# Kernel tuning notes

Hardware: AMD Instinct MI355X
Metric: run time of the kernel (lower is better)

Reference implementation:

```python
import jax, jax.numpy as jnp
import numpy as np

B, T, D = 4, 2048, 2048
H = 16
HO = D // H  # head_out = 128


def setup_inputs() -> dict:
    key = jax.random.key(0)
    ks = jax.random.split(key, 6)
    x = jax.random.normal(ks[0], (B, T, D), dtype=jnp.float32)
    scale = 0.02
    Wq = jax.random.normal(ks[1], (D, D), dtype=jnp.float32) * scale
    Wk = jax.random.normal(ks[2], (D, D), dtype=jnp.float32) * scale
    Wv = jax.random.normal(ks[3], (D, D), dtype=jnp.float32) * scale
    Wp = jax.random.normal(ks[4], (D, D), dtype=jnp.float32) * scale
    bp = jnp.zeros((D,), dtype=jnp.float32)
    return {"x": x, "Wq": Wq, "Wk": Wk, "Wv": Wv, "Wp": Wp, "bp": bp}


def reference(x, Wq, Wk, Wv, Wp, bp):
    b, t, _ = x.shape
    # QKV projections (weights stored [d_in, d_out])
    q = x @ Wq
    k = x @ Wk
    v = x @ Wv
    split = lambda a: a.reshape(b, t, H, HO).transpose(0, 2, 1, 3)  # [b,H,T,ho]
    qh, kh, vh = split(q), split(k), split(v)
    # Feature attention: contract over tokens -> [b,H,ho,ho]
    scores = jnp.einsum('bhtf,bhtg->bhfg', qh, kh) / jnp.sqrt(jnp.float32(HO))
    weights = jax.nn.softmax(scores, axis=-1)  # dropout p=0.0 (identity)
    # feature_alibi: [1/T, 1/(T-1), ..., 1], broadcast over batch/head/feature
    feat_alibi = (1.0 / jnp.arange(t, 0, -1, dtype=jnp.float32)).reshape(1, 1, t, 1)
    vh = vh + feat_alibi
    # (weights @ v^T)^T : ctx[b,h,t,f] = sum_g weights[b,h,f,g] * v[b,h,t,g]
    ctx = jnp.einsum('bhfg,bhtg->bhtf', weights, vh)
    ctx = ctx.transpose(0, 2, 1, 3).reshape(b, t, H * HO)  # [b,T,d_out]
    return ctx @ Wp + bp
```

## Files before the change

### kernel.cpp

```cpp
#include <hip/hip_runtime.h>
#include <hip/hip_bf16.h>


#define Tt 2048
#define Dd 2048
#define Mm 8192

typedef __attribute__((ext_vector_type(4))) float f32x4;
typedef __attribute__((ext_vector_type(8))) short s16x8;
static_assert(sizeof(s16x8) == 16, "frag size");

typedef const __attribute__((address_space(1))) void* gptr_t;
typedef __attribute__((address_space(3))) void* lptr_t;

__device__ __forceinline__ float bf2f(ushort u) {
    union { unsigned int i; float f; } c; c.i = ((unsigned int)u) << 16; return c.f;
}
__device__ __forceinline__ ushort f2bf(float f) {
    union { float f; unsigned int i; } c; c.f = f;
    return (ushort)((c.i + 0x7FFFu + ((c.i >> 16) & 1u)) >> 16);
}
__device__ __forceinline__ void gload16(const void* g, void* l) {
    __builtin_amdgcn_global_load_lds((gptr_t)g, (lptr_t)l, 16, 0, 0);
}
__device__ __forceinline__ s16x8 ldfrag(const char* p) { return *(const s16x8*)p; }

#define MFMA_BF16(d, a, b) \
    asm("v_mfma_f32_16x16x32_bf16 %0, %1, %2, %0" : "+v"(d) : "v"(a), "v"(b))


__global__ __launch_bounds__(256) void convx_kernel(const float* __restrict__ x,
                                                    ushort* __restrict__ xb) {
    const int idx = blockIdx.x * 256 + threadIdx.x;
    const int stride = gridDim.x * 256;
    for (int i = idx; i < Mm * Dd / 4; i += stride) {
        const float4 v = *(const float4*)(x + (size_t)i * 4);
        ushort4 o; o.x = f2bf(v.x); o.y = f2bf(v.y); o.z = f2bf(v.z); o.w = f2bf(v.w);
        *(ushort4*)(xb + (size_t)i * 4) = o;
    }
}

__global__ __launch_bounds__(256) void transw_kernel(const float* __restrict__ W0,
        const float* __restrict__ W1, const float* __restrict__ W2,
        const float* __restrict__ W3, ushort* __restrict__ Wt) {
    __shared__ float tile[64][65];
    const int z = blockIdx.z;
    const float* W = (z == 0) ? W0 : (z == 1) ? W1 : (z == 2) ? W2 : W3;
    ushort* dst = Wt + (size_t)z * ((size_t)Dd * Dd);
    const int n0 = blockIdx.x * 64, k0 = blockIdx.y * 64;
    const int r4 = threadIdx.x >> 6, c = threadIdx.x & 63;
#pragma unroll
    for (int i = 0; i < 16; i++) {
        const int row = i * 4 + r4;
        tile[row][c] = W[(size_t)(k0 + row) * Dd + n0 + c];
    }
    __syncthreads();
#pragma unroll
    for (int i = 0; i < 16; i++) {
        const int row = i * 4 + r4;
        dst[(size_t)(n0 + row) * Dd + k0 + c] = f2bf(tile[c][row]);
    }
}


__device__ __forceinline__ void stage_half(char* ldsRegion, const ushort* gRegion,
                                           int ld, int half, int tid) {
#pragma unroll
    for (int j = 0; j < 2; j++) {
        const int Pb = half * 16384 + j * 8192 + (tid >> 6) * 1024;
        const int P = Pb + (tid & 63) * 16;
        const int row = P >> 7;
        const int colb = (P ^ ((row & 7) << 4)) & 127;
        gload16(gRegion + (size_t)row * ld + (colb >> 1), ldsRegion + Pb);
    }
}

template <int MODE>
__global__ __launch_bounds__(512, 2) void gemm256_kernel(
        const ushort* __restrict__ A, const ushort* __restrict__ Bt,
        void* __restrict__ Cv, const float* __restrict__ bias,
        int Kdim, int lda, int ldb, int ldc,
        size_t bstride, size_t cstride) {
    extern __shared__ char lds[];

    const int tid = threadIdx.x;
    const int lane = tid & 63;
    const int w = tid >> 6;
    const int wr = w >> 2, wc = w & 3;
    const int fr = lane & 15, fq = lane >> 4;

    const int bid = blockIdx.x;
    const int wg = (bid & 7) * 32 + (bid >> 3);
    const int m0 = (wg >> 3) * 256;
    const int n0 = (wg & 7) * 256;

    const ushort* Ag = A + (size_t)m0 * lda;
    const ushort* Bg = Bt + (size_t)blockIdx.z * bstride + (size_t)n0 * ldb;
    const int NT = Kdim >> 6;

    const int aoff = wr * 16384 + fr * 128;
    const int boff = wc * 8192 + fr * 128;
    const int xo = (fr & 7) << 4;
    const int cp0 = (fq * 16) ^ xo;
    const int cp1 = (64 + fq * 16) ^ xo;

    f32x4 acc[8][4];
#pragma unroll
    for (int i = 0; i < 8; i++)
#pragma unroll
        for (int j = 0; j < 4; j++) acc[i][j] = {0.f, 0.f, 0.f, 0.f};

    s16x8 afX[4][2], afY[4][2], bf01[2][2], bf23[2][2];

    {
        char* b0 = lds;
        char* b1 = lds + 65536;
        stage_half(b0,         Ag, lda, 0, tid);
        stage_half(b0,         Ag, lda, 1, tid);
        stage_half(b0 + 32768, Bg, ldb, 0, tid);
        stage_half(b0 + 32768, Bg, ldb, 1, tid);
        if (NT > 1) {
            stage_half(b1, Ag + 64, lda, 0, tid);
            stage_half(b1, Ag + 64, lda, 1, tid);
        }
        __builtin_amdgcn_sched_barrier(0);
        if (NT > 1) asm volatile("s_waitcnt vmcnt(4)" ::: "memory");
        else        asm volatile("s_waitcnt vmcnt(0)" ::: "memory");
        __builtin_amdgcn_s_barrier();
        const char* Ab = b0 + aoff;
        const char* Bb = b0 + 32768 + boff;
#pragma unroll
        for (int m = 0; m < 4; m++) {
            afX[m][0] = ldfrag(Ab + m * 2048 + cp0);
            afX[m][1] = ldfrag(Ab + m * 2048 + cp1);
        }
#pragma unroll
        for (int n = 0; n < 2; n++) {
            bf01[n][0] = ldfrag(Bb + n * 2048 + cp0);
            bf01[n][1] = ldfrag(Bb + n * 2048 + cp1);
        }
        __builtin_amdgcn_sched_barrier(0);
    }

    for (int t = 0; t < NT; ++t) {
        char* bufc = lds + (t & 1) * 65536;
        char* bufn = lds + ((t & 1) ^ 1) * 65536;
        const char* Ab = bufc + aoff;
        const char* Bb = bufc + 32768 + boff;

#pragma unroll
        for (int n = 0; n < 2; n++) {
            bf23[n][0] = ldfrag(Bb + (n + 2) * 2048 + cp0);
            bf23[n][1] = ldfrag(Bb + (n + 2) * 2048 + cp1);
        }
        if (t + 1 < NT) stage_half(bufn + 32768, Bg + (size_t)(t + 1) * 64, ldb, 0, tid);
        __builtin_amdgcn_sched_barrier(0);
        __builtin_amdgcn_s_barrier();
        asm volatile("s_waitcnt lgkmcnt(4)" ::: "memory");
        __builtin_amdgcn_s_setprio(1);
#pragma unroll
        for (int k = 0; k < 2; k++)
#pragma unroll
            for (int m = 0; m < 4; m++)
#pragma unroll
                for (int n = 0; n < 2; n++) MFMA_BF16(acc[m][n], afX[m][k], bf01[n][k]);
        __builtin_amdgcn_s_setprio(0);
        __builtin_amdgcn_s_barrier();

#pragma unroll
        for (int m = 0; m < 4; m++) {
            afY[m][0] = ldfrag(Ab + (m + 4) * 2048 + cp0);
            afY[m][1] = ldfrag(Ab + (m + 4) * 2048 + cp1);
        }
        if (t + 1 < NT) stage_half(bufn + 32768, Bg + (size_t)(t + 1) * 64, ldb, 1, tid);
        __builtin_amdgcn_sched_barrier(0);
        __builtin_amdgcn_s_barrier();
        asm volatile("s_waitcnt lgkmcnt(8)" ::: "memory");
        __builtin_amdgcn_s_setprio(1);
#pragma unroll
        for (int k = 0; k < 2; k++)
#pragma unroll
            for (int m = 0; m < 4; m++)
#pragma unroll
                for (int n = 0; n < 2; n++) MFMA_BF16(acc[m][n + 2], afX[m][k], bf23[n][k]);
        __builtin_amdgcn_s_setprio(0);
        __builtin_amdgcn_s_barrier();

        asm volatile("s_waitcnt lgkmcnt(0)" ::: "memory");
        __builtin_amdgcn_s_setprio(1);
#pragma unroll
        for (int k = 0; k < 2; k++)
#pragma unroll
            for (int m = 0; m < 4; m++)
#pragma unroll
                for (int n = 0; n < 2; n++) MFMA_BF16(acc[m + 4][n], afY[m][k], bf01[n][k]);
        __builtin_amdgcn_s_setprio(0);
        __builtin_amdgcn_s_barrier();

        if (t + 2 < NT) {
            stage_half(bufc, Ag + (size_t)(t + 2) * 64, lda, 0, tid);
            stage_half(bufc, Ag + (size_t)(t + 2) * 64, lda, 1, tid);
        }
        __builtin_amdgcn_sched_barrier(0);
        if (t + 2 < NT) asm volatile("s_waitcnt vmcnt(4)" ::: "memory");
        else            asm volatile("s_waitcnt vmcnt(0)" ::: "memory");
        __builtin_amdgcn_s_barrier();
        if (t + 1 < NT) {
            const char* nAb = bufn + aoff;
            const char* nBb = bufn + 32768 + boff;
#pragma unroll
            for (int m = 0; m < 4; m++) {
                afX[m][0] = ldfrag(nAb + m * 2048 + cp0);
                afX[m][1] = ldfrag(nAb + m * 2048 + cp1);
            }
#pragma unroll
            for (int n = 0; n < 2; n++) {
                bf01[n][0] = ldfrag(nBb + n * 2048 + cp0);
                bf01[n][1] = ldfrag(nBb + n * 2048 + cp1);
            }
        }
        __builtin_amdgcn_sched_barrier(0);
        __builtin_amdgcn_s_setprio(1);
#pragma unroll
        for (int k = 0; k < 2; k++)
#pragma unroll
            for (int m = 0; m < 4; m++)
#pragma unroll
                for (int n = 0; n < 2; n++) MFMA_BF16(acc[m + 4][n + 2], afY[m][k], bf23[n][k]);
        __builtin_amdgcn_s_setprio(0);
        __builtin_amdgcn_s_barrier();
    }

    asm volatile("s_nop 7\ns_nop 7\ns_nop 7");

    if (MODE == 2) {
        float* C = (float*)Cv;
#pragma unroll
        for (int mi = 0; mi < 8; mi++)
#pragma unroll
            for (int ni = 0; ni < 4; ni++)
#pragma unroll
                for (int r = 0; r < 4; r++) {
                    const int row = m0 + wr * 128 + mi * 16 + fq * 4 + r;
                    const int col = n0 + wc * 64 + ni * 16 + fr;
                    C[(size_t)row * ldc + col] = acc[mi][ni][r] + bias[col];
                }
    } else {
        ushort* C = (ushort*)Cv + (size_t)blockIdx.z * cstride;
#pragma unroll
        for (int mi = 0; mi < 8; mi++)
#pragma unroll
            for (int ni = 0; ni < 4; ni++)
#pragma unroll
                for (int r = 0; r < 4; r++) {
                    const int row = m0 + wr * 128 + mi * 16 + fq * 4 + r;
                    const int col = n0 + wc * 64 + ni * 16 + fr;
                    C[(size_t)row * ldc + col] = f2bf(acc[mi][ni][r]);
                }
    }
}


template <int MODE>
__global__ __launch_bounds__(256, 2) void gemm_kernel(
        const ushort* __restrict__ A, const ushort* __restrict__ Bt,
        void* __restrict__ Cv, const float* __restrict__ bias,
        int Kdim, int lda, int ldb, int ldc) {
    __shared__ ushort lsA[128 * 32];
    __shared__ ushort lsB[128 * 32];

    const int tid = threadIdx.x;
    const int w = tid >> 6, lane = tid & 63;
    const int m0 = blockIdx.y * 128;
    const int n0 = blockIdx.x * 128;

    const ushort* Ab = A;
    const ushort* Bb = Bt;
    size_t coff = 0;
    if (MODE == 1) {
        const int z = blockIdx.z, b = z >> 4, h = z & 15;
        const size_t ao = (size_t)b * ((size_t)Tt * Dd) + (size_t)h * 128;
        Ab += ao; Bb += (size_t)z * (128 * 128); coff = ao;
    }

    const int sr = lane >> 2;
    const int sc = (lane & 3) * 8;
    const int c0 = w, c1 = w + 4;
    const int rA0 = c0 * 16 + sr, rA1 = c1 * 16 + sr;

    const int fr = lane & 15, fq = lane >> 4;
    const int wr = (w >> 1) * 64, wc = (w & 1) * 64;

    f32x4 acc[4][4];
#pragma unroll
    for (int i = 0; i < 4; i++)
#pragma unroll
        for (int j = 0; j < 4; j++) acc[i][j] = {0.f, 0.f, 0.f, 0.f};

    for (int kt = 0; kt < Kdim; kt += 32) {
        gload16(Ab + (size_t)(m0 + rA0) * lda + kt + sc, lsA + c0 * 512);
        gload16(Ab + (size_t)(m0 + rA1) * lda + kt + sc, lsA + c1 * 512);
        gload16(Bb + (size_t)(n0 + rA0) * ldb + kt + sc, lsB + c0 * 512);
        gload16(Bb + (size_t)(n0 + rA1) * ldb + kt + sc, lsB + c1 * 512);
        __syncthreads();

        s16x8 afrag[4], bfrag[4];
#pragma unroll
        for (int i = 0; i < 4; i++)
            afrag[i] = *(const s16x8*)(lsA + (wr + i * 16 + fr) * 32 + fq * 8);
#pragma unroll
        for (int j = 0; j < 4; j++)
            bfrag[j] = *(const s16x8*)(lsB + (wc + j * 16 + fr) * 32 + fq * 8);
#pragma unroll
        for (int i = 0; i < 4; i++)
#pragma unroll
            for (int j = 0; j < 4; j++)
                MFMA_BF16(acc[i][j], afrag[i], bfrag[j]);
        __syncthreads();
    }

    asm volatile("s_nop 7\ns_nop 7\ns_nop 7");

    {
        ushort* C = (ushort*)Cv + coff;
#pragma unroll
        for (int i = 0; i < 4; i++)
#pragma unroll
            for (int j = 0; j < 4; j++)
#pragma unroll
                for (int r = 0; r < 4; r++) {
                    const int row = m0 + wr + i * 16 + fq * 4 + r;
                    const int col = n0 + wc + j * 16 + fr;
                    float val = acc[i][j][r];
                    if (MODE == 1) val += 1.0f / (float)(Tt - row);
                    C[(size_t)row * ldc + col] = f2bf(val);
                }
    }
}


__global__ __launch_bounds__(256) void scores_kernel(const ushort* __restrict__ q,
        const ushort* __restrict__ k, float* __restrict__ part) {
    __shared__ float lsQ[32][128];
    __shared__ float lsK[32][128];
    const int tid = threadIdx.x;
    const int s = blockIdx.x, bh = blockIdx.y;
    const int b = bh >> 4, h = bh & 15;
    const size_t base = (size_t)b * ((size_t)Tt * Dd) + (size_t)h * 128;
    const ushort* qb = q + base;
    const ushort* kb = k + base;
    const int ty = tid >> 4, tx = tid & 15;
    const int f0 = ty * 8, g0 = tx * 8;

    float acc[8][8];
#pragma unroll
    for (int i = 0; i < 8; i++)
#pragma unroll
        for (int j = 0; j < 8; j++) acc[i][j] = 0.f;

    for (int ch = 0; ch < 8; ch++) {
        const int t0 = s * 256 + ch * 32;
#pragma unroll
        for (int ii = 0; ii < 4; ii++) {
            const int e = ii * 1024 + tid * 4;
            const int r = e >> 7, cc = e & 127;
            const size_t ga = (size_t)(t0 + r) * Dd + cc;
            const ushort4 v4 = *(const ushort4*)(qb + ga);
            f32x4 qf = {bf2f(v4.x), bf2f(v4.y), bf2f(v4.z), bf2f(v4.w)};
            *(f32x4*)&lsQ[r][cc] = qf;
            const ushort4 w4 = *(const ushort4*)(kb + ga);
            f32x4 kf = {bf2f(w4.x), bf2f(w4.y), bf2f(w4.z), bf2f(w4.w)};
            *(f32x4*)&lsK[r][cc] = kf;
        }
        __syncthreads();
#pragma unroll 4
        for (int tl = 0; tl < 32; tl++) {
            float qv[8], kv[8];
            *(f32x4*)&qv[0] = *(const f32x4*)&lsQ[tl][f0];
            *(f32x4*)&qv[4] = *(const f32x4*)&lsQ[tl][f0 + 4];
            *(f32x4*)&kv[0] = *(const f32x4*)&lsK[tl][g0];
            *(f32x4*)&kv[4] = *(const f32x4*)&lsK[tl][g0 + 4];
#pragma unroll
            for (int i = 0; i < 8; i++)
#pragma unroll
                for (int j = 0; j < 8; j++)
                    acc[i][j] = fmaf(qv[i], kv[j], acc[i][j]);
        }
        __syncthreads();
    }
    float* pb = part + ((size_t)s * 64 + bh) * 16384;
#pragma unroll
    for (int i = 0; i < 8; i++) {
        f32x4 o0 = {acc[i][0], acc[i][1], acc[i][2], acc[i][3]};
        f32x4 o1 = {acc[i][4], acc[i][5], acc[i][6], acc[i][7]};
        *(f32x4*)&pb[(f0 + i) * 128 + g0] = o0;
        *(f32x4*)&pb[(f0 + i) * 128 + g0 + 4] = o1;
    }
}


__global__ __launch_bounds__(256) void softmax_kernel(const float* __restrict__ part,
                                                      ushort* __restrict__ wts) {
    const int tid = threadIdx.x;
    const int wv = tid >> 6, lane = tid & 63;
    const int row = blockIdx.x * 4 + wv;
    const float* p = part + (size_t)row * 128 + lane * 2;
    float v0 = 0.f, v1 = 0.f;
#pragma unroll
    for (int s = 0; s < 8; s++) {
        const float2 t = *(const float2*)(p + (size_t)s * 1048576);
        v0 += t.x; v1 += t.y;
    }
    const float sc = 0.088388347648318447f;
    v0 *= sc; v1 *= sc;
    float m = fmaxf(v0, v1);
#pragma unroll
    for (int off = 32; off > 0; off >>= 1) m = fmaxf(m, __shfl_xor(m, off));
    const float e0 = __expf(v0 - m), e1 = __expf(v1 - m);
    float smv = e0 + e1;
#pragma unroll
    for (int off = 32; off > 0; off >>= 1) smv += __shfl_xor(smv, off);
    const float inv = 1.0f / smv;
    ushort2 o; o.x = f2bf(e0 * inv); o.y = f2bf(e1 * inv);
    *(ushort2*)(wts + (size_t)row * 128 + lane * 2) = o;
}


extern "C" void kernel_launch(void* const* d_in, const int* in_sizes, int n_in,
                              void* d_out, int out_size, void* d_ws, size_t ws_size,
                              hipStream_t stream) {
    const float* x  = (const float*)d_in[0];
    const float* Wq = (const float*)d_in[1];
    const float* Wk = (const float*)d_in[2];
    const float* Wv = (const float*)d_in[3];
    const float* Wp = (const float*)d_in[4];
    const float* bp = (const float*)d_in[5];
    float* out = (float*)d_out;
    char* ws = (char*)d_ws;

    ushort* xb   = (ushort*)(ws);
    ushort* Wt   = (ushort*)(ws + (33ull << 20));
    ushort* q    = (ushort*)(ws + (65ull << 20));
    ushort* k    = (ushort*)(ws + (97ull << 20));
    ushort* v    = (ushort*)(ws + (129ull << 20));
    float*  part = (float*) (ws + (161ull << 20));
    ushort* wts  = (ushort*)(ws + (193ull << 20));
    ushort* ctx  = xb;

    const size_t WSZ = (size_t)Dd * Dd;
    const size_t QSTRIDE = (32ull << 20) / 2;

    static_cast<void>(hipFuncSetAttribute((const void*)gemm256_kernel<0>,
        hipFuncAttributeMaxDynamicSharedMemorySize, 131072));
    static_cast<void>(hipFuncSetAttribute((const void*)gemm256_kernel<2>,
        hipFuncAttributeMaxDynamicSharedMemorySize, 131072));

    convx_kernel<<<2048, 256, 0, stream>>>(x, xb);
    transw_kernel<<<dim3(32, 32, 4), 256, 0, stream>>>(Wq, Wk, Wv, Wp, Wt);

    gemm256_kernel<0><<<dim3(256, 1, 3), 512, 131072, stream>>>(
        xb, Wt, q, nullptr, 2048, 2048, 2048, 2048, WSZ, QSTRIDE);

    scores_kernel<<<dim3(8, 64), 256, 0, stream>>>(q, k, part);
    softmax_kernel<<<2048, 256, 0, stream>>>(part, wts);

    gemm_kernel<1><<<dim3(1, 16, 64), 256, 0, stream>>>(v, wts, ctx, nullptr, 128, 2048, 128, 2048);

    gemm256_kernel<2><<<dim3(256, 1, 1), 512, 131072, stream>>>(
        ctx, Wt + 3 * WSZ, out, bp, 2048, 2048, 2048, 2048, 0, 0);
}
```

Baseline: 370.6 us.

## Restructure GEMM main loop to prefetch both A and B two tiles ahead

Changes the software pipeline of the bf16 MFMA GEMM so that both A and B tiles are staged into LDS two iterations ahead, instead of prefetching B only one iteration ahead. The per-iteration fragment loads for afX/bf01 move to the top of the loop rather than being issued at the end of the previous iteration. The vmcnt waits are adjusted to match the deeper prefetch. The aim is to hide more global-load latency. The cost is less overlap between LDS fragment reads and the MFMA blocks, since there are extra lgkmcnt(0) waits and barriers.

Result: no change. 376.8 us (+1.7%).

```diff
diff --git a/kernel.cpp b/kernel.cpp
--- a/kernel.cpp
+++ b/kernel.cpp
@@ -120,15 +120,24 @@
         stage_half(b0 + 32768, Bg, ldb, 0, tid);
         stage_half(b0 + 32768, Bg, ldb, 1, tid);
         if (NT > 1) {
-            stage_half(b1, Ag + 64, lda, 0, tid);
-            stage_half(b1, Ag + 64, lda, 1, tid);
-        }
-        __builtin_amdgcn_sched_barrier(0);
-        if (NT > 1) asm volatile("s_waitcnt vmcnt(4)" ::: "memory");
+            stage_half(b1,         Ag + 64, lda, 0, tid);
+            stage_half(b1,         Ag + 64, lda, 1, tid);
+            stage_half(b1 + 32768, Bg + 64, ldb, 0, tid);
+            stage_half(b1 + 32768, Bg + 64, ldb, 1, tid);
+        }
+        __builtin_amdgcn_sched_barrier(0);
+        if (NT > 1) asm volatile("s_waitcnt vmcnt(8)" ::: "memory");
         else        asm volatile("s_waitcnt vmcnt(0)" ::: "memory");
         __builtin_amdgcn_s_barrier();
-        const char* Ab = b0 + aoff;
-        const char* Bb = b0 + 32768 + boff;
+    }
+
+    for (int t = 0; t < NT; ++t) {
+        char* bufc = lds + (t & 1) * 65536;
+        const char* Ab = bufc + aoff;
+        const char* Bb = bufc + 32768 + boff;
+        const ushort* Ag2 = Ag + (size_t)(t + 2) * 64;
+        const ushort* Bg2 = Bg + (size_t)(t + 2) * 64;
+
 #pragma unroll
         for (int m = 0; m < 4; m++) {
             afX[m][0] = ldfrag(Ab + m * 2048 + cp0);
@@ -140,30 +149,36 @@
             bf01[n][1] = ldfrag(Bb + n * 2048 + cp1);
         }
         __builtin_amdgcn_sched_barrier(0);
-    }
-
-    for (int t = 0; t < NT; ++t) {
-        char* bufc = lds + (t & 1) * 65536;
-        char* bufn = lds + ((t & 1) ^ 1) * 65536;
-        const char* Ab = bufc + aoff;
-        const char* Bb = bufc + 32768 + boff;
+        asm volatile("s_waitcnt lgkmcnt(8)" ::: "memory");
+        __builtin_amdgcn_s_barrier();
+        asm volatile("s_waitcnt lgkmcnt(0)" ::: "memory");
+        __builtin_amdgcn_sched_barrier(0);
+        __builtin_amdgcn_s_setprio(1);
+#pragma unroll
+        for (int k = 0; k < 2; k++)
+#pragma unroll
+            for (int m = 0; m < 4; m++)
+#pragma unroll
+                for (int n = 0; n < 2; n++) MFMA_BF16(acc[m][n], afX[m][k], bf01[n][k]);
+        __builtin_amdgcn_s_setprio(0);
+        __builtin_amdgcn_s_barrier();
 
 #pragma unroll
         for (int n = 0; n < 2; n++) {
             bf23[n][0] = ldfrag(Bb + (n + 2) * 2048 + cp0);
             bf23[n][1] = ldfrag(Bb + (n + 2) * 2048 + cp1);
         }
-        if (t + 1 < NT) stage_half(bufn + 32768, Bg + (size_t)(t + 1) * 64, ldb, 0, tid);
-        __builtin_amdgcn_sched_barrier(0);
-        __builtin_amdgcn_s_barrier();
-        asm volatile("s_waitcnt lgkmcnt(4)" ::: "memory");
+        __builtin_amdgcn_sched_barrier(0);
+        __builtin_amdgcn_s_barrier();
+        asm volatile("s_waitcnt lgkmcnt(0)" ::: "memory");
+        __builtin_amdgcn_sched_barrier(0);
         __builtin_amdgcn_s_setprio(1);
 #pragma unroll
         for (int k = 0; k < 2; k++)
 #pragma unroll
             for (int m = 0; m < 4; m++)
 #pragma unroll
-                for (int n = 0; n < 2; n++) MFMA_BF16(acc[m][n], afX[m][k], bf01[n][k]);
+                for (int n = 0; n < 2; n++) MFMA_BF16(acc[m][n + 2], afX[m][k], bf23[n][k]);
         __builtin_amdgcn_s_setprio(0);
         __builtin_amdgcn_s_barrier();
 
@@ -172,21 +187,14 @@
             afY[m][0] = ldfrag(Ab + (m + 4) * 2048 + cp0);
             afY[m][1] = ldfrag(Ab + (m + 4) * 2048 + cp1);
         }
-        if (t + 1 < NT) stage_half(bufn + 32768, Bg + (size_t)(t + 1) * 64, ldb, 1, tid);
-        __builtin_amdgcn_sched_barrier(0);
-        __builtin_amdgcn_s_barrier();
-        asm volatile("s_waitcnt lgkmcnt(8)" ::: "memory");
-        __builtin_amdgcn_s_setprio(1);
-#pragma unroll
-        for (int k = 0; k < 2; k++)
-#pragma unroll
-            for (int m = 0; m < 4; m++)
-#pragma unroll
-                for (int n = 0; n < 2; n++) MFMA_BF16(acc[m][n + 2], afX[m][k], bf23[n][k]);
-        __builtin_amdgcn_s_setprio(0);
-        __builtin_amdgcn_s_barrier();
-
+        if (t + 2 < NT) {
+            stage_half(bufc + 32768, Bg2, ldb, 0, tid);
+            stage_half(bufc + 32768, Bg2, ldb, 1, tid);
+        }
+        __builtin_amdgcn_sched_barrier(0);
+        __builtin_amdgcn_s_barrier();
         asm volatile("s_waitcnt lgkmcnt(0)" ::: "memory");
+        __builtin_amdgcn_sched_barrier(0);
         __builtin_amdgcn_s_setprio(1);
 #pragma unroll
         for (int k = 0; k < 2; k++)
@@ -198,28 +206,13 @@
         __builtin_amdgcn_s_barrier();
 
         if (t + 2 < NT) {
-            stage_half(bufc, Ag + (size_t)(t + 2) * 64, lda, 0, tid);
-            stage_half(bufc, Ag + (size_t)(t + 2) * 64, lda, 1, tid);
-        }
-        __builtin_amdgcn_sched_barrier(0);
-        if (t + 2 < NT) asm volatile("s_waitcnt vmcnt(4)" ::: "memory");
+            stage_half(bufc, Ag2, lda, 0, tid);
+            stage_half(bufc, Ag2, lda, 1, tid);
+        }
+        __builtin_amdgcn_sched_barrier(0);
+        if (t + 2 < NT) asm volatile("s_waitcnt vmcnt(8)" ::: "memory");
         else            asm volatile("s_waitcnt vmcnt(0)" ::: "memory");
         __builtin_amdgcn_s_barrier();
-        if (t + 1 < NT) {
-            const char* nAb = bufn + aoff;
-            const char* nBb = bufn + 32768 + boff;
-#pragma unroll
-            for (int m = 0; m < 4; m++) {
-                afX[m][0] = ldfrag(nAb + m * 2048 + cp0);
-                afX[m][1] = ldfrag(nAb + m * 2048 + cp1);
-            }
-#pragma unroll
-            for (int n = 0; n < 2; n++) {
-                bf01[n][0] = ldfrag(nBb + n * 2048 + cp0);
-                bf01[n][1] = ldfrag(nBb + n * 2048 + cp1);
-            }
-        }
-        __builtin_amdgcn_sched_barrier(0);
         __builtin_amdgcn_s_setprio(1);
 #pragma unroll
         for (int k = 0; k < 2; k++)
```
